# Performance work log

Measured on AMD Instinct MI355X. Metric: run time of the kernel, lower is better.

Reference implementation:

```python
import jax, jax.numpy as jnp
import numpy as np

RANKS_HIGH = 15   # dt.RANKS.HIGH in the repo
SUITS_HIGH = 14   # padded so conv output last dim == 10 (Linear(10,32))
EPS = 1e-5


def _bn(x, g, b, axes):
    # Batch-norm over `axes` with channel dim = 1, training-mode batch stats.
    m = jnp.mean(x, axis=axes, keepdims=True)
    v = jnp.var(x, axis=axes, keepdims=True)
    xn = (x - m) * jax.lax.rsqrt(v + EPS)
    shp = [1] * x.ndim
    shp[1] = -1
    return xn * g.reshape(shp) + b.reshape(shp)


def setup_inputs() -> dict:
    key = jax.random.key(0)
    ks = jax.random.split(key, 16)
    M = 4096
    s = 0.05
    return {
        "x": jax.random.randint(ks[0], (M, 5, 2), 0, 4),  # (rank, suit) indices
        "conv_w": jax.random.normal(ks[1], (64, 5, 5, 5), jnp.float32) * s,
        "conv_b": jax.random.normal(ks[2], (64,), jnp.float32) * s,
        "bn0_g": jnp.ones((64,), jnp.float32),
        "bn0_b": jnp.zeros((64,), jnp.float32),
        "w_rank": jax.random.normal(ks[3], (32, 10), jnp.float32) * s,
        "b_rank": jax.random.normal(ks[4], (32,), jnp.float32) * s,
        "w_h1": jax.random.normal(ks[5], (32, 32), jnp.float32) * s,
        "b_h1": jax.random.normal(ks[6], (32,), jnp.float32) * s,
        "bn1_g": jnp.ones((64,), jnp.float32),
        "bn1_b": jnp.zeros((64,), jnp.float32),
        "w_h2": jax.random.normal(ks[7], (16, 32), jnp.float32) * s,
        "b_h2": jax.random.normal(ks[8], (16,), jnp.float32) * s,
        "bn2_g": jnp.ones((64,), jnp.float32),
        "bn2_b": jnp.zeros((64,), jnp.float32),
        "w_out": jax.random.normal(ks[9], (9, 11264), jnp.float32) * s,
        "b_out": jax.random.normal(ks[10], (9,), jnp.float32) * s,
    }


def reference(x, conv_w, conv_b, bn0_g, bn0_b, w_rank, b_rank, w_h1, b_h1,
              bn1_g, bn1_b, w_h2, b_h2, bn2_g, bn2_b, w_out, b_out):
    ranks = x[:, :, 0]
    suits = x[:, :, 1]
    # Vectorized replacement of the double Python-loop one-hot scatter:
    # three_d[j, i, ranks[j, i], suits[j, i]] = 1  ->  outer product of one-hots.
    three_d = (jax.nn.one_hot(ranks, RANKS_HIGH, dtype=jnp.float32)[..., :, None]
               * jax.nn.one_hot(suits, SUITS_HIGH, dtype=jnp.float32)[..., None, :])  # [M,5,15,14]
    r = jax.lax.conv_general_dilated(
        three_d, conv_w, window_strides=(1, 1), padding="VALID",
        dimension_numbers=("NCHW", "OIHW", "NCHW"))  # [M,64,11,10]
    r = r + conv_b[None, :, None, None]
    r = jax.nn.relu(_bn(r, bn0_g, bn0_b, (0, 2, 3)))
    r = jax.nn.relu(jnp.einsum("mchs,os->mcho", r, w_rank) + b_rank)      # [M,64,11,32]
    r = jnp.einsum("mchi,oi->mcho", r, w_h1) + b_h1                        # [M,64,11,32]
    r = jax.nn.relu(_bn(r, bn1_g, bn1_b, (0, 2, 3)))
    r = jnp.einsum("mchi,oi->mcho", r, w_h2) + b_h2                        # [M,64,11,16]
    r = jax.nn.relu(_bn(r, bn2_g, bn2_b, (0, 2, 3)))
    r = r.reshape(r.shape[0], -1)                                          # [M,11264]
    return r @ w_out.T + b_out                                             # [M,9]
```

## Files before the change

kernel.cpp:

```cpp
#include <hip/hip_runtime.h>
#include <hip/hip_bf16.h>

#define EPSV 1e-5f

typedef float vf2 __attribute__((ext_vector_type(2)));
typedef _Float16 h4f __attribute__((ext_vector_type(4)));

__device__ __forceinline__ vf2 pk_fma(vf2 a, vf2 b, vf2 c) {
  vf2 d;
  asm("v_pk_fma_f32 %0, %1, %2, %3" : "=v"(d) : "v"(a), "v"(b), "v"(c));
  return d;
}
__device__ __forceinline__ vf2 pk_mul(vf2 a, vf2 b) {
  vf2 d;
  asm("v_pk_mul_f32 %0, %1, %2" : "=v"(d) : "v"(a), "v"(b));
  return d;
}

#define WS_SUM0   0
#define WS_SSQ0   64
#define WS_SUM1   128
#define WS_SSQ1   192
#define WS_SUM2   256
#define WS_SSQ2   320
#define WS_AL0    384
#define WS_BE0    448
#define WS_ZBG    512
#define WS_T1BG   576
#define WS_AL1    2624
#define WS_BE1    2688
#define WS_T2BG   2752
#define WS_AL2    3776
#define WS_BE2    3840
#define WS_A2BG   3904
#define WS_OC     4928
#define WS_CU     4992
#define WS_CW     5120
#define WS_HIST   10304
#define WS_WSUM   13056
#define WS_T1     24576

#define CONV_LDS 5184
#define NHIST 2640

__device__ __forceinline__ void stage_conv(float* sW, const float* __restrict__ conv_w,
                                           int nthr) {
  for (int i = threadIdx.x; i < 8000; i += nthr) {
    int k = i / 125, rem = i - k * 125;
    int cc = rem / 25, r2 = rem - cc * 25;
    int di = r2 / 5, dj = r2 - di * 5;
    if (di < 4 && dj < 4) sW[k * 81 + cc * 16 + di * 4 + dj] = conv_w[i];
  }
  for (int k = threadIdx.x; k < 64; k += nthr) sW[k * 81 + 80] = 0.f;
}

__device__ __forceinline__ void stage_conv_fast(float* sW, const float* __restrict__ cw) {
  const float4* src = (const float4*)cw;
  float4* dst = (float4*)sW;
  for (int i = threadIdx.x; i < CONV_LDS / 4; i += 256) dst[i] = src[i];
}

__device__ __forceinline__ int conv_idx(int di, int dj, int cc) {
  int idx = cc * 16 + di * 4 + dj;
  return ((di | dj) >= 0) ? idx : 80;
}

__global__ __launch_bounds__(256) void k_prep3(
    const int* __restrict__ x, const float* __restrict__ conv_w,
    const float* __restrict__ w_out, float* __restrict__ ws, int M) {
  __shared__ float h[NHIST];
  const int b = blockIdx.x;
  const int tid = threadIdx.x;
  if (b < 8) {
    float* cw = ws + WS_CW;
    const int gid = b * 256 + tid;
    for (int i = gid; i < 8000; i += 8 * 256) {
      int k = i / 125, rem = i - k * 125;
      int cc = rem / 25, r2 = rem - cc * 25;
      int di = r2 / 5, dj = r2 - di * 5;
      if (di < 4 && dj < 4) cw[k * 81 + cc * 16 + di * 4 + dj] = conv_w[i];
    }
    for (int k = gid; k < 64; k += 8 * 256) cw[k * 81 + 80] = 0.f;
  } else if (b < 44) {
    const int gid = (b - 8) * 256 + tid;
    if (gid < 9216) {
      int j = gid / 1024, kp = gid - j * 1024;
      int k = kp >> 4, p = kp & 15;
      float s = 0.f;
#pragma unroll
      for (int yy = 4; yy < 11; ++yy)
        s += w_out[j * 11264 + k * 176 + yy * 16 + p];
      ws[WS_WSUM + gid] = s;
    }
  } else {
    for (int i = tid; i < NHIST; i += 256) h[i] = 0.f;
    __syncthreads();
    for (int m = (b - 44) * 256 + tid; m < M; m += 16 * 256) {
      int v[5];
      const int2* xp = (const int2*)(x + m * 10);
#pragma unroll
      for (int cc = 0; cc < 5; ++cc) {
        int2 t = xp[cc];
        v[cc] = (t.x << 2) | t.y;
      }
#pragma unroll
      for (int cc = 0; cc < 5; ++cc) atomicAdd(&h[cc * 16 + v[cc]], 1.f);
      int pr = 0;
#pragma unroll
      for (int a = 0; a < 5; ++a)
#pragma unroll
        for (int bb = a + 1; bb < 5; ++bb) {
          atomicAdd(&h[80 + pr * 256 + v[a] * 16 + v[bb]], 1.f);
          ++pr;
        }
    }
    __syncthreads();
    for (int i = tid; i < NHIST; i += 256)
      if (h[i] != 0.f) atomicAdd(&ws[WS_HIST + i], h[i]);
  }
}

__global__ __launch_bounds__(256) void k_stats0h(
    const float* __restrict__ conv_b, float* __restrict__ ws, int M) {
  __shared__ float sWk[81];
  const int tid = threadIdx.x;
  const int k = blockIdx.x;
  if (tid < 81) sWk[tid] = ws[WS_CW + k * 81 + tid];
  __syncthreads();
  const float cb = conv_b[k];
  const float* H = ws + WS_HIST;
  float L = 0.f, Q = 0.f, P = 0.f;
  for (int it = tid; it < 1280; it += 256) {
    int pos = it / 80, rem = it - pos * 80;
    int cc = rem >> 4, v = rem & 15;
    int y = pos >> 2, xx = pos & 3;
    float w = sWk[conv_idx((v >> 2) - y, (v & 3) - xx, cc)];
    float n = H[cc * 16 + v];
    L += n * w;
    Q += n * w * w;
  }
  if (tid < 160) {
    int pos = tid / 10, pr = tid - pos * 10;
    int y = pos >> 2, xx = pos & 3;
    int a, b;
    if (pr < 4)      { a = 0; b = pr + 1; }
    else if (pr < 7) { a = 1; b = pr - 2; }
    else if (pr < 9) { a = 2; b = pr - 4; }
    else             { a = 3; b = 4; }
    const float* Hp = H + 80 + pr * 256;
    for (int v1 = 0; v1 < 16; ++v1) {
      float w1 = sWk[conv_idx((v1 >> 2) - y, (v1 & 3) - xx, a)];
      float acc = 0.f;
#pragma unroll
      for (int v2 = 0; v2 < 16; ++v2) {
        float w2 = sWk[conv_idx((v2 >> 2) - y, (v2 & 3) - xx, b)];
        acc += Hp[v1 * 16 + v2] * w2;
      }
      P += w1 * acc;
    }
  }
  atomicAdd(&ws[WS_SUM0 + k], L);
  atomicAdd(&ws[WS_SSQ0 + k], Q + 2.f * cb * L + 2.f * P);
  if (tid == 0) {
    const float a16 = 16.f * (float)M;
    atomicAdd(&ws[WS_SUM0 + k], a16 * cb);
    atomicAdd(&ws[WS_SSQ0 + k], a16 * cb * cb);
  }
}

__global__ __launch_bounds__(64) void k_fin0(
    const float* __restrict__ conv_b, const float* __restrict__ g0,
    const float* __restrict__ b0, const float* __restrict__ w_rank,
    const float* __restrict__ b_rank, const float* __restrict__ w_h1,
    const float* __restrict__ b_h1, float* __restrict__ ws, int M) {
  __shared__ float sS[32];
  const int t = threadIdx.x;
  if (t < 32) {
    float su = 0.f;
    for (int s2 = 0; s2 < 10; ++s2) su += w_rank[t * 10 + s2];
    sS[t] = su;
    float cu = 0.f;
    for (int s2 = 4; s2 < 10; ++s2) cu += w_rank[t * 10 + s2];
    ws[WS_CU + t] = cu;
  }
  __syncthreads();
  const int k = t;
  const float n0 = 110.f * (float)M;
  const float cb = conv_b[k];
  const float S  = ws[WS_SUM0 + k] + 94.f * (float)M * cb;
  const float SS = ws[WS_SSQ0 + k] + 94.f * (float)M * cb * cb;
  const float mu = S / n0;
  const float var = SS / n0 - mu * mu;
  const float rstd = rsqrtf(var + EPSV);
  const float al = rstd * g0[k];
  const float be = b0[k] - mu * al;
  ws[WS_AL0 + k] = al;
  ws[WS_BE0 + k] = be;
  const float zbg = fmaxf(cb * al + be, 0.f);
  ws[WS_ZBG + k] = zbg;
  float r1bg[32];
#pragma unroll
  for (int o = 0; o < 32; ++o) r1bg[o] = fmaxf(zbg * sS[o] + b_rank[o], 0.f);
  float sb = 0.f, ssb = 0.f;
  for (int o = 0; o < 32; ++o) {
    float acc = b_h1[o];
#pragma unroll
    for (int i = 0; i < 32; ++i) acc += r1bg[i] * w_h1[o * 32 + i];
    ws[WS_T1BG + k * 32 + o] = acc;
    sb += acc;
    ssb += acc * acc;
  }
  ws[WS_SUM1 + k] = 7.f * (float)M * sb;
  ws[WS_SSQ1 + k] = 7.f * (float)M * ssb;
}

__global__ __launch_bounds__(256) void k_t1(
    const int* __restrict__ x, const float* __restrict__ conv_b,
    const float* __restrict__ w_rank, const float* __restrict__ b_rank,
    const float* __restrict__ w_h1, const float* __restrict__ b_h1,
    float* __restrict__ ws, float* __restrict__ t1, int M) {
  __shared__ float sW[CONV_LDS];
  stage_conv_fast(sW, ws + WS_CW);
  __syncthreads();
  const int tid = threadIdx.x;
  const int y = tid & 3, k = tid >> 2;
  const float cb = conv_b[k];
  const float al = ws[WS_AL0 + k], be = ws[WS_BE0 + k], zbg = ws[WS_ZBG + k];
  const float* Wk = &sW[k * 81];
  const float* cu = ws + WS_CU;
  const vf2* wrp = (const vf2*)w_rank;
  const vf2* w1p = (const vf2*)w_h1;
  h4f* t1h = (h4f*)t1;
  float sAcc = 0.f, ssAcc = 0.f;
  const int NP = (M + 1) >> 1;
  for (int mp = blockIdx.x; mp < NP; mp += gridDim.x) {
    const int mA = mp * 2, mB = mA + 1;
    const bool hasB = (mB < M);
    const int mBs = hasB ? mB : mA;
    int rA[5], cA[5], rB[5], cBx[5];
    const int2* xpA = (const int2*)(x + mA * 10);
    const int2* xpB = (const int2*)(x + mBs * 10);
#pragma unroll
    for (int cc = 0; cc < 5; ++cc) {
      int2 tA = xpA[cc]; rA[cc] = tA.x; cA[cc] = tA.y;
      int2 tB = xpB[cc]; rB[cc] = tB.x; cBx[cc] = tB.y;
    }
    float a0A[4], a0B[4];
#pragma unroll
    for (int xx = 0; xx < 4; ++xx) {
      float vA = cb, vB = cb;
#pragma unroll
      for (int cc = 0; cc < 5; ++cc) {
        vA += Wk[conv_idx(rA[cc] - y, cA[cc] - xx, cc)];
        vB += Wk[conv_idx(rB[cc] - y, cBx[cc] - xx, cc)];
      }
      a0A[xx] = fmaxf(al * vA + be, 0.f);
      a0B[xx] = fmaxf(al * vB + be, 0.f);
    }
    vf2 aAp[2], aBp[2];
    aAp[0].x = a0A[0]; aAp[0].y = a0A[1];
    aAp[1].x = a0A[2]; aAp[1].y = a0A[3];
    aBp[0].x = a0B[0]; aBp[0].y = a0B[1];
    aBp[1].x = a0B[2]; aBp[1].y = a0B[3];
    __builtin_amdgcn_sched_barrier(0);
    vf2 r1A[16], r1B[16];
#pragma unroll
    for (int o2 = 0; o2 < 16; ++o2) {
      const int oa = 2 * o2, ob = oa + 1;
      vf2 w0 = wrp[oa * 5], w1 = wrp[oa * 5 + 1];
      vf2 w2 = wrp[ob * 5], w3 = wrp[ob * 5 + 1];
      const float basea = b_rank[oa] + zbg * cu[oa];
      const float baseb = b_rank[ob] + zbg * cu[ob];
      vf2 accAa = pk_mul(aAp[0], w0); accAa = pk_fma(aAp[1], w1, accAa);
      vf2 accAb = pk_mul(aAp[0], w2); accAb = pk_fma(aAp[1], w3, accAb);
      vf2 accBa = pk_mul(aBp[0], w0); accBa = pk_fma(aBp[1], w1, accBa);
      vf2 accBb = pk_mul(aBp[0], w2); accBb = pk_fma(aBp[1], w3, accBb);
      vf2 ra, rb;
      ra.x = fmaxf(basea + accAa.x + accAa.y, 0.f);
      ra.y = fmaxf(baseb + accAb.x + accAb.y, 0.f);
      rb.x = fmaxf(basea + accBa.x + accBa.y, 0.f);
      rb.y = fmaxf(baseb + accBb.x + accBb.y, 0.f);
      r1A[o2] = ra;
      r1B[o2] = rb;
    }
    __builtin_amdgcn_sched_barrier(0);
    float sBm = 0.f, ssBm = 0.f;
#pragma unroll
    for (int chv = 0; chv < 8; ++chv) {
      float accA[4], accB[4];
#pragma unroll
      for (int u = 0; u < 4; ++u) {
        const int o = chv * 4 + u;
        vf2 a2A = {0.f, 0.f}, a2B = {0.f, 0.f};
#pragma unroll
        for (int i = 0; i < 16; ++i) {
          vf2 w = w1p[o * 16 + i];
          a2A = pk_fma(r1A[i], w, a2A);
          a2B = pk_fma(r1B[i], w, a2B);
        }
        const float bb = b_h1[o];
        float aA = bb + a2A.x + a2A.y;
        float aB = bb + a2B.x + a2B.y;
        accA[u] = aA; accB[u] = aB;
        sAcc += aA; ssAcc += aA * aA;
        sBm += aB;  ssBm += aB * aB;
      }
      h4f stA;
      stA[0] = (_Float16)accA[0]; stA[1] = (_Float16)accA[1];
      stA[2] = (_Float16)accA[2]; stA[3] = (_Float16)accA[3];
      t1h[((size_t)mA * 8 + chv) * 256 + tid] = stA;
      if (hasB) {
        h4f stB;
        stB[0] = (_Float16)accB[0]; stB[1] = (_Float16)accB[1];
        stB[2] = (_Float16)accB[2]; stB[3] = (_Float16)accB[3];
        t1h[((size_t)mB * 8 + chv) * 256 + tid] = stB;
      }
      __builtin_amdgcn_sched_barrier(0);
    }
    if (hasB) { sAcc += sBm; ssAcc += ssBm; }
  }
  sAcc  += __shfl_xor(sAcc, 1);  sAcc  += __shfl_xor(sAcc, 2);
  ssAcc += __shfl_xor(ssAcc, 1); ssAcc += __shfl_xor(ssAcc, 2);
  if (y == 0) {
    atomicAdd(&ws[WS_SUM1 + k], sAcc);
    atomicAdd(&ws[WS_SSQ1 + k], ssAcc);
  }
}

__global__ __launch_bounds__(64) void k_fin1(
    const float* __restrict__ g1, const float* __restrict__ b1,
    const float* __restrict__ w_h2, const float* __restrict__ b_h2,
    float* __restrict__ ws, int M) {
  const int k = threadIdx.x;
  const float n1 = (float)M * 11.f * 32.f;
  const float S = ws[WS_SUM1 + k], SS = ws[WS_SSQ1 + k];
  const float mu = S / n1;
  const float var = SS / n1 - mu * mu;
  const float rstd = rsqrtf(var + EPSV);
  const float al = rstd * g1[k];
  const float be = b1[k] - mu * al;
  ws[WS_AL1 + k] = al;
  ws[WS_BE1 + k] = be;
  float a1bg[32];
#pragma unroll
  for (int o = 0; o < 32; ++o)
    a1bg[o] = fmaxf(al * ws[WS_T1BG + k * 32 + o] + be, 0.f);
  float sb = 0.f, ssb = 0.f;
  for (int p = 0; p < 16; ++p) {
    float acc = b_h2[p];
#pragma unroll
    for (int o = 0; o < 32; ++o) acc += a1bg[o] * w_h2[p * 32 + o];
    ws[WS_T2BG + k * 16 + p] = acc;
    sb += acc;
    ssb += acc * acc;
  }
  ws[WS_SUM2 + k] = 7.f * (float)M * sb;
  ws[WS_SSQ2 + k] = 7.f * (float)M * ssb;
}

__global__ __launch_bounds__(256) void k_t2(
    const float* __restrict__ w_h2, const float* __restrict__ b_h2,
    float* __restrict__ ws, float* __restrict__ t1, int M) {
  const int tid = threadIdx.x;
  const int y = tid & 3, k = tid >> 2;
  const float al1 = ws[WS_AL1 + k], be1 = ws[WS_BE1 + k];
  const vf2* w2p = (const vf2*)w_h2;
  h4f* t1h = (h4f*)t1;
  float sAcc = 0.f, ssAcc = 0.f;
  const int NP = (M + 1) >> 1;
  for (int mp = blockIdx.x; mp < NP; mp += gridDim.x) {
    const int mA = mp * 2, mB = mA + 1;
    const bool hasB = (mB < M);
    const int mBs = hasB ? mB : mA;
    vf2 a1A[16], a1B[16];
#pragma unroll
    for (int chv = 0; chv < 8; ++chv) {
      h4f vA = t1h[((size_t)mA * 8 + chv) * 256 + tid];
      h4f vB = t1h[((size_t)mBs * 8 + chv) * 256 + tid];
      vf2 pA0, pA1, pB0, pB1;
      pA0.x = fmaxf(al1 * (float)vA[0] + be1, 0.f);
      pA0.y = fmaxf(al1 * (float)vA[1] + be1, 0.f);
      pA1.x = fmaxf(al1 * (float)vA[2] + be1, 0.f);
      pA1.y = fmaxf(al1 * (float)vA[3] + be1, 0.f);
      pB0.x = fmaxf(al1 * (float)vB[0] + be1, 0.f);
      pB0.y = fmaxf(al1 * (float)vB[1] + be1, 0.f);
      pB1.x = fmaxf(al1 * (float)vB[2] + be1, 0.f);
      pB1.y = fmaxf(al1 * (float)vB[3] + be1, 0.f);
      a1A[chv * 2] = pA0; a1A[chv * 2 + 1] = pA1;
      a1B[chv * 2] = pB0; a1B[chv * 2 + 1] = pB1;
    }
    __builtin_amdgcn_sched_barrier(0);
    float sBm = 0.f, ssBm = 0.f;
#pragma unroll
    for (int pv = 0; pv < 4; ++pv) {
      float accA[4], accB[4];
#pragma unroll
      for (int u = 0; u < 4; ++u) {
        const int p = pv * 4 + u;
        vf2 a2A = {0.f, 0.f}, a2B = {0.f, 0.f};
#pragma unroll
        for (int i = 0; i < 16; ++i) {
          vf2 w = w2p[p * 16 + i];
          a2A = pk_fma(a1A[i], w, a2A);
          a2B = pk_fma(a1B[i], w, a2B);
        }
        const float bb = b_h2[p];
        float aA = bb + a2A.x + a2A.y;
        float aB = bb + a2B.x + a2B.y;
        accA[u] = aA; accB[u] = aB;
        sAcc += aA; ssAcc += aA * aA;
        sBm += aB;  ssBm += aB * aB;
      }
      h4f stA;
      stA[0] = (_Float16)accA[0]; stA[1] = (_Float16)accA[1];
      stA[2] = (_Float16)accA[2]; stA[3] = (_Float16)accA[3];
      t1h[((size_t)mA * 8 + pv) * 256 + tid] = stA;
      if (hasB) {
        h4f stB;
        stB[0] = (_Float16)accB[0]; stB[1] = (_Float16)accB[1];
        stB[2] = (_Float16)accB[2]; stB[3] = (_Float16)accB[3];
        t1h[((size_t)mB * 8 + pv) * 256 + tid] = stB;
      }
      __builtin_amdgcn_sched_barrier(0);
    }
    if (hasB) { sAcc += sBm; ssAcc += ssBm; }
  }
  sAcc  += __shfl_xor(sAcc, 1);  sAcc  += __shfl_xor(sAcc, 2);
  ssAcc += __shfl_xor(ssAcc, 1); ssAcc += __shfl_xor(ssAcc, 2);
  if (y == 0) {
    atomicAdd(&ws[WS_SUM2 + k], sAcc);
    atomicAdd(&ws[WS_SSQ2 + k], ssAcc);
  }
}

__global__ __launch_bounds__(64) void k_fin2f(
    const float* __restrict__ g2, const float* __restrict__ b2,
    const float* __restrict__ b_out, float* __restrict__ ws, int M) {
  __shared__ float red[64 * 9];
  const int k = threadIdx.x;
  const float n2 = (float)M * 11.f * 16.f;
  const float S = ws[WS_SUM2 + k], SS = ws[WS_SSQ2 + k];
  const float mu = S / n2;
  const float var = SS / n2 - mu * mu;
  const float rstd = rsqrtf(var + EPSV);
  const float al = rstd * g2[k];
  const float be = b2[k] - mu * al;
  ws[WS_AL2 + k] = al;
  ws[WS_BE2 + k] = be;
  float a2bg[16];
#pragma unroll
  for (int p = 0; p < 16; ++p) {
    a2bg[p] = fmaxf(al * ws[WS_T2BG + k * 16 + p] + be, 0.f);
    ws[WS_A2BG + k * 16 + p] = a2bg[p];
  }
  for (int j = 0; j < 9; ++j) {
    const float* wsj = ws + WS_WSUM + j * 1024 + k * 16;
    float acc = 0.f;
#pragma unroll
    for (int p = 0; p < 16; ++p) acc += a2bg[p] * wsj[p];
    red[k * 9 + j] = acc;
  }
  __syncthreads();
  if (k < 9) {
    float acc = b_out[k];
    for (int t = 0; t < 64; ++t) acc += red[t * 9 + k];
    ws[WS_OC + k] = acc;
  }
}

__global__ __launch_bounds__(256) void k_out(
    const float* __restrict__ w_out, const float* __restrict__ ws,
    const float* __restrict__ t1, float* __restrict__ out, int M) {
  __shared__ float sOC[9];
  __shared__ float sRedA[4][9], sRedB[4][9];
  if (threadIdx.x < 9) sOC[threadIdx.x] = ws[WS_OC + threadIdx.x];
  __syncthreads();
  const int tid = threadIdx.x;
  const int lane = tid & 63, wv = tid >> 6;
  const int y = tid & 3, k = tid >> 2;
  const float al2 = ws[WS_AL2 + k], be2 = ws[WS_BE2 + k];
  const float4* wo = (const float4*)(w_out + k * 176 + y * 16);
  const h4f* t2h = (const h4f*)t1;
  const int NP = (M + 1) >> 1;
  bool first = true;
  for (int mp = blockIdx.x; mp < NP; mp += gridDim.x) {
    if (!first) __syncthreads();
    first = false;
    const int mA = mp * 2, mB = mA + 1;
    const bool hasB = (mB < M);
    const int mBs = hasB ? mB : mA;
    vf2 a2A[8], a2B[8];
#pragma unroll
    for (int iv = 0; iv < 4; ++iv) {
      h4f vA = t2h[((size_t)mA * 8 + iv) * 256 + tid];
      h4f vB = t2h[((size_t)mBs * 8 + iv) * 256 + tid];
      vf2 pA0, pA1, pB0, pB1;
      pA0.x = fmaxf(al2 * (float)vA[0] + be2, 0.f);
      pA0.y = fmaxf(al2 * (float)vA[1] + be2, 0.f);
      pA1.x = fmaxf(al2 * (float)vA[2] + be2, 0.f);
      pA1.y = fmaxf(al2 * (float)vA[3] + be2, 0.f);
      pB0.x = fmaxf(al2 * (float)vB[0] + be2, 0.f);
      pB0.y = fmaxf(al2 * (float)vB[1] + be2, 0.f);
      pB1.x = fmaxf(al2 * (float)vB[2] + be2, 0.f);
      pB1.y = fmaxf(al2 * (float)vB[3] + be2, 0.f);
      a2A[iv * 2] = pA0; a2A[iv * 2 + 1] = pA1;
      a2B[iv * 2] = pB0; a2B[iv * 2 + 1] = pB1;
    }
    float poA[9], poB[9];
#pragma unroll
    for (int j = 0; j < 9; ++j) {
      float4 w0 = wo[j * 2816 + 0], w1 = wo[j * 2816 + 1];
      float4 w2 = wo[j * 2816 + 2], w3 = wo[j * 2816 + 3];
      vf2 aA = {0.f, 0.f}, aB = {0.f, 0.f};
      vf2 t;
      t.x = w0.x; t.y = w0.y; aA = pk_fma(a2A[0], t, aA); aB = pk_fma(a2B[0], t, aB);
      t.x = w0.z; t.y = w0.w; aA = pk_fma(a2A[1], t, aA); aB = pk_fma(a2B[1], t, aB);
      t.x = w1.x; t.y = w1.y; aA = pk_fma(a2A[2], t, aA); aB = pk_fma(a2B[2], t, aB);
      t.x = w1.z; t.y = w1.w; aA = pk_fma(a2A[3], t, aA); aB = pk_fma(a2B[3], t, aB);
      t.x = w2.x; t.y = w2.y; aA = pk_fma(a2A[4], t, aA); aB = pk_fma(a2B[4], t, aB);
      t.x = w2.z; t.y = w2.w; aA = pk_fma(a2A[5], t, aA); aB = pk_fma(a2B[5], t, aB);
      t.x = w3.x; t.y = w3.y; aA = pk_fma(a2A[6], t, aA); aB = pk_fma(a2B[6], t, aB);
      t.x = w3.z; t.y = w3.w; aA = pk_fma(a2A[7], t, aA); aB = pk_fma(a2B[7], t, aB);
      poA[j] = aA.x + aA.y;
      poB[j] = aB.x + aB.y;
    }
#pragma unroll
    for (int j = 0; j < 9; ++j) {
      float vA = poA[j], vB = poB[j];
      vA += __shfl_xor(vA, 1);  vB += __shfl_xor(vB, 1);
      vA += __shfl_xor(vA, 2);  vB += __shfl_xor(vB, 2);
      vA += __shfl_xor(vA, 4);  vB += __shfl_xor(vB, 4);
      vA += __shfl_xor(vA, 8);  vB += __shfl_xor(vB, 8);
      vA += __shfl_xor(vA, 16); vB += __shfl_xor(vB, 16);
      vA += __shfl_xor(vA, 32); vB += __shfl_xor(vB, 32);
      poA[j] = vA; poB[j] = vB;
    }
    if (lane == 0) {
#pragma unroll
      for (int j = 0; j < 9; ++j) { sRedA[wv][j] = poA[j]; sRedB[wv][j] = poB[j]; }
    }
    __syncthreads();
    if (tid < 9) {
      float acc = sOC[tid];
#pragma unroll
      for (int w2i = 0; w2i < 4; ++w2i) acc += sRedA[w2i][tid];
      out[mA * 9 + tid] = acc;
    } else if (tid >= 64 && tid < 73 && hasB) {
      const int j = tid - 64;
      float acc = sOC[j];
#pragma unroll
      for (int w2i = 0; w2i < 4; ++w2i) acc += sRedB[w2i][j];
      out[mB * 9 + j] = acc;
    }
  }
}

__global__ __launch_bounds__(256) void k_stats0(
    const int* __restrict__ x, const float* __restrict__ conv_w,
    const float* __restrict__ conv_b, float* __restrict__ ws, int M) {
  __shared__ float sW[CONV_LDS];
  stage_conv(sW, conv_w, 256);
  __syncthreads();
  const int tid = threadIdx.x;
  const int mg = tid & 3;
  const int k  = tid >> 2;
  const float cb = conv_b[k];
  const float* Wk = &sW[k * 81];
  float s = 0.f, ss = 0.f;
  for (int m = blockIdx.x * 4 + mg; m < M; m += gridDim.x * 4) {
    int r[5], c[5];
    const int2* xp = (const int2*)(x + m * 10);
#pragma unroll
    for (int cc = 0; cc < 5; ++cc) { int2 t = xp[cc]; r[cc] = t.x; c[cc] = t.y; }
#pragma unroll
    for (int y = 0; y < 4; ++y) {
#pragma unroll
      for (int xx = 0; xx < 4; ++xx) {
        float v = cb;
#pragma unroll
        for (int cc = 0; cc < 5; ++cc)
          v += Wk[conv_idx(r[cc] - y, c[cc] - xx, cc)];
        s += v;
        ss += v * v;
      }
      __builtin_amdgcn_sched_barrier(0);
    }
  }
  s  += __shfl_xor(s, 1);  s  += __shfl_xor(s, 2);
  ss += __shfl_xor(ss, 1); ss += __shfl_xor(ss, 2);
  if (mg == 0) {
    atomicAdd(&ws[WS_SUM0 + k], s);
    atomicAdd(&ws[WS_SSQ0 + k], ss);
  }
}

__global__ __launch_bounds__(256) void k_stats1(
    const int* __restrict__ x, const float* __restrict__ conv_w,
    const float* __restrict__ conv_b, const float* __restrict__ w_rank,
    const float* __restrict__ b_rank, const float* __restrict__ w_h1,
    const float* __restrict__ b_h1, float* __restrict__ ws, int M) {
  __shared__ float sW[CONV_LDS];
  stage_conv(sW, conv_w, 256);
  __syncthreads();
  const int tid = threadIdx.x;
  const int y = tid & 3, k = tid >> 2;
  const float cb = conv_b[k];
  const float al = ws[WS_AL0 + k], be = ws[WS_BE0 + k], zbg = ws[WS_ZBG + k];
  const float* Wk = &sW[k * 81];
  const float* cu = ws + WS_CU;
  float sAcc = 0.f, ssAcc = 0.f;
  for (int m = blockIdx.x; m < M; m += gridDim.x) {
    int r[5], c[5];
    const int2* xp = (const int2*)(x + m * 10);
#pragma unroll
    for (int cc = 0; cc < 5; ++cc) { int2 t = xp[cc]; r[cc] = t.x; c[cc] = t.y; }
    float a0[4];
#pragma unroll
    for (int xx = 0; xx < 4; ++xx) {
      float v = cb;
#pragma unroll
      for (int cc = 0; cc < 5; ++cc)
        v += Wk[conv_idx(r[cc] - y, c[cc] - xx, cc)];
      a0[xx] = fmaxf(al * v + be, 0.f);
    }
    __builtin_amdgcn_sched_barrier(0);
    float r1[32];
#pragma unroll
    for (int o = 0; o < 32; ++o) {
      float acc = b_rank[o] + zbg * cu[o];
#pragma unroll
      for (int xx = 0; xx < 4; ++xx) acc += a0[xx] * w_rank[o * 10 + xx];
      r1[o] = fmaxf(acc, 0.f);
    }
    __builtin_amdgcn_sched_barrier(0);
    float s1 = 0.f, ss1 = 0.f;
#pragma unroll
    for (int ch = 0; ch < 4; ++ch) {
#pragma unroll
      for (int u = 0; u < 8; ++u) {
        const int o = ch * 8 + u;
        float acc = b_h1[o];
#pragma unroll
        for (int i = 0; i < 32; ++i) acc += r1[i] * w_h1[o * 32 + i];
        s1 += acc;
        ss1 += acc * acc;
      }
      __builtin_amdgcn_sched_barrier(0);
    }
    sAcc += s1;
    ssAcc += ss1;
  }
  sAcc  += __shfl_xor(sAcc, 1);  sAcc  += __shfl_xor(sAcc, 2);
  ssAcc += __shfl_xor(ssAcc, 1); ssAcc += __shfl_xor(ssAcc, 2);
  if (y == 0) {
    atomicAdd(&ws[WS_SUM1 + k], sAcc);
    atomicAdd(&ws[WS_SSQ1 + k], ssAcc);
  }
}

__global__ __launch_bounds__(256) void k_stats2(
    const int* __restrict__ x, const float* __restrict__ conv_w,
    const float* __restrict__ conv_b, const float* __restrict__ w_rank,
    const float* __restrict__ b_rank, const float* __restrict__ w_h1,
    const float* __restrict__ b_h1, const float* __restrict__ w_h2,
    const float* __restrict__ b_h2, float* __restrict__ ws, int M) {
  __shared__ float sW[CONV_LDS];
  stage_conv(sW, conv_w, 256);
  __syncthreads();
  const int tid = threadIdx.x;
  const int y = tid & 3, k = tid >> 2;
  const float cb = conv_b[k];
  const float al = ws[WS_AL0 + k], be = ws[WS_BE0 + k], zbg = ws[WS_ZBG + k];
  const float al1 = ws[WS_AL1 + k], be1 = ws[WS_BE1 + k];
  const float* Wk = &sW[k * 81];
  const float* cu = ws + WS_CU;
  float sAcc = 0.f, ssAcc = 0.f;
  for (int m = blockIdx.x; m < M; m += gridDim.x) {
    int r[5], c[5];
    const int2* xp = (const int2*)(x + m * 10);
#pragma unroll
    for (int cc = 0; cc < 5; ++cc) { int2 t = xp[cc]; r[cc] = t.x; c[cc] = t.y; }
    float a0[4];
#pragma unroll
    for (int xx = 0; xx < 4; ++xx) {
      float v = cb;
#pragma unroll
      for (int cc = 0; cc < 5; ++cc)
        v += Wk[conv_idx(r[cc] - y, c[cc] - xx, cc)];
      a0[xx] = fmaxf(al * v + be, 0.f);
    }
    __builtin_amdgcn_sched_barrier(0);
    float r1[32];
#pragma unroll
    for (int o = 0; o < 32; ++o) {
      float acc = b_rank[o] + zbg * cu[o];
#pragma unroll
      for (int xx = 0; xx < 4; ++xx) acc += a0[xx] * w_rank[o * 10 + xx];
      r1[o] = fmaxf(acc, 0.f);
    }
    __builtin_amdgcn_sched_barrier(0);
    float t2[16];
#pragma unroll
    for (int p = 0; p < 16; ++p) t2[p] = b_h2[p];
#pragma unroll
    for (int ch = 0; ch < 4; ++ch) {
      float a1c[8];
#pragma unroll
      for (int u = 0; u < 8; ++u) {
        const int o = ch * 8 + u;
        float acc = b_h1[o];
#pragma unroll
        for (int i = 0; i < 32; ++i) acc += r1[i] * w_h1[o * 32 + i];
        a1c[u] = fmaxf(al1 * acc + be1, 0.f);
      }
      __builtin_amdgcn_sched_barrier(0);
#pragma unroll
      for (int p = 0; p < 16; ++p) {
        float acc = t2[p];
#pragma unroll
        for (int u = 0; u < 8; ++u) acc += a1c[u] * w_h2[p * 32 + ch * 8 + u];
        t2[p] = acc;
      }
      __builtin_amdgcn_sched_barrier(0);
    }
    float s2l = 0.f, ss2l = 0.f;
#pragma unroll
    for (int p = 0; p < 16; ++p) { s2l += t2[p]; ss2l += t2[p] * t2[p]; }
    sAcc += s2l;
    ssAcc += ss2l;
  }
  sAcc  += __shfl_xor(sAcc, 1);  sAcc  += __shfl_xor(sAcc, 2);
  ssAcc += __shfl_xor(ssAcc, 1); ssAcc += __shfl_xor(ssAcc, 2);
  if (y == 0) {
    atomicAdd(&ws[WS_SUM2 + k], sAcc);
    atomicAdd(&ws[WS_SSQ2 + k], ssAcc);
  }
}

__global__ __launch_bounds__(64) void k_fin2(
    const float* __restrict__ g2, const float* __restrict__ b2,
    const float* __restrict__ w_out, const float* __restrict__ b_out,
    float* __restrict__ ws, int M) {
  __shared__ float red[64 * 9];
  const int k = threadIdx.x;
  const float n2 = (float)M * 11.f * 16.f;
  const float S = ws[WS_SUM2 + k], SS = ws[WS_SSQ2 + k];
  const float mu = S / n2;
  const float var = SS / n2 - mu * mu;
  const float rstd = rsqrtf(var + EPSV);
  const float al = rstd * g2[k];
  const float be = b2[k] - mu * al;
  ws[WS_AL2 + k] = al;
  ws[WS_BE2 + k] = be;
  float a2bg[16];
#pragma unroll
  for (int p = 0; p < 16; ++p) {
    a2bg[p] = fmaxf(al * ws[WS_T2BG + k * 16 + p] + be, 0.f);
    ws[WS_A2BG + k * 16 + p] = a2bg[p];
  }
  for (int j = 0; j < 9; ++j) {
    float acc = 0.f;
#pragma unroll
    for (int p = 0; p < 16; ++p) {
      float wsum = 0.f;
#pragma unroll
      for (int yy = 4; yy < 11; ++yy)
        wsum += w_out[j * 11264 + k * 176 + yy * 16 + p];
      acc += a2bg[p] * wsum;
    }
    red[k * 9 + j] = acc;
  }
  __syncthreads();
  if (k < 9) {
    float acc = b_out[k];
    for (int t = 0; t < 64; ++t) acc += red[t * 9 + k];
    ws[WS_OC + k] = acc;
  }
}

__global__ __launch_bounds__(256) void k_final(
    const int* __restrict__ x, const float* __restrict__ conv_w,
    const float* __restrict__ conv_b, const float* __restrict__ w_rank,
    const float* __restrict__ b_rank, const float* __restrict__ w_h1,
    const float* __restrict__ b_h1, const float* __restrict__ w_h2,
    const float* __restrict__ b_h2, const float* __restrict__ w_out,
    const float* __restrict__ ws, float* __restrict__ out, int M) {
  __shared__ float sW[CONV_LDS];
  __shared__ float sOC[9];
  __shared__ float sRed[4][9];
  stage_conv(sW, conv_w, 256);
  if (threadIdx.x < 9) sOC[threadIdx.x] = ws[WS_OC + threadIdx.x];
  __syncthreads();
  const int tid = threadIdx.x;
  const int lane = tid & 63, wv = tid >> 6;
  const int y = tid & 3, k = tid >> 2;
  const float cb = conv_b[k];
  const float al = ws[WS_AL0 + k], be = ws[WS_BE0 + k], zbg = ws[WS_ZBG + k];
  const float al1 = ws[WS_AL1 + k], be1 = ws[WS_BE1 + k];
  const float al2 = ws[WS_AL2 + k], be2 = ws[WS_BE2 + k];
  const float* Wk = &sW[k * 81];
  const float* cu = ws + WS_CU;
  const float4* wo = (const float4*)(w_out + k * 176 + y * 16);
  bool first = true;
  for (int m = blockIdx.x; m < M; m += gridDim.x) {
    if (!first) __syncthreads();
    first = false;
    int r[5], c[5];
    const int2* xp = (const int2*)(x + m * 10);
#pragma unroll
    for (int cc = 0; cc < 5; ++cc) { int2 t = xp[cc]; r[cc] = t.x; c[cc] = t.y; }
    float a0[4];
#pragma unroll
    for (int xx = 0; xx < 4; ++xx) {
      float v = cb;
#pragma unroll
      for (int cc = 0; cc < 5; ++cc)
        v += Wk[conv_idx(r[cc] - y, c[cc] - xx, cc)];
      a0[xx] = fmaxf(al * v + be, 0.f);
    }
    __builtin_amdgcn_sched_barrier(0);
    float r1[32];
#pragma unroll
    for (int o = 0; o < 32; ++o) {
      float acc = b_rank[o] + zbg * cu[o];
#pragma unroll
      for (int xx = 0; xx < 4; ++xx) acc += a0[xx] * w_rank[o * 10 + xx];
      r1[o] = fmaxf(acc, 0.f);
    }
    __builtin_amdgcn_sched_barrier(0);
    float t2[16];
#pragma unroll
    for (int p = 0; p < 16; ++p) t2[p] = b_h2[p];
#pragma unroll
    for (int ch = 0; ch < 4; ++ch) {
      float a1c[8];
#pragma unroll
      for (int u = 0; u < 8; ++u) {
        const int o = ch * 8 + u;
        float acc = b_h1[o];
#pragma unroll
        for (int i = 0; i < 32; ++i) acc += r1[i] * w_h1[o * 32 + i];
        a1c[u] = fmaxf(al1 * acc + be1, 0.f);
      }
      __builtin_amdgcn_sched_barrier(0);
#pragma unroll
      for (int p = 0; p < 16; ++p) {
        float acc = t2[p];
#pragma unroll
        for (int u = 0; u < 8; ++u) acc += a1c[u] * w_h2[p * 32 + ch * 8 + u];
        t2[p] = acc;
      }
      __builtin_amdgcn_sched_barrier(0);
    }
    float a2[16];
#pragma unroll
    for (int p = 0; p < 16; ++p) a2[p] = fmaxf(al2 * t2[p] + be2, 0.f);
    float po[9];
#pragma unroll
    for (int j = 0; j < 9; ++j) {
      float4 w0 = wo[j * 2816 + 0], w1 = wo[j * 2816 + 1];
      float4 w2 = wo[j * 2816 + 2], w3 = wo[j * 2816 + 3];
      po[j] = a2[0] * w0.x + a2[1] * w0.y + a2[2] * w0.z + a2[3] * w0.w
            + a2[4] * w1.x + a2[5] * w1.y + a2[6] * w1.z + a2[7] * w1.w
            + a2[8] * w2.x + a2[9] * w2.y + a2[10] * w2.z + a2[11] * w2.w
            + a2[12] * w3.x + a2[13] * w3.y + a2[14] * w3.z + a2[15] * w3.w;
    }
#pragma unroll
    for (int j = 0; j < 9; ++j) {
      float v = po[j];
      v += __shfl_xor(v, 1);
      v += __shfl_xor(v, 2);
      v += __shfl_xor(v, 4);
      v += __shfl_xor(v, 8);
      v += __shfl_xor(v, 16);
      v += __shfl_xor(v, 32);
      po[j] = v;
    }
    if (lane == 0) {
#pragma unroll
      for (int j = 0; j < 9; ++j) sRed[wv][j] = po[j];
    }
    __syncthreads();
    if (tid < 9) {
      float acc = sOC[tid];
#pragma unroll
      for (int w2i = 0; w2i < 4; ++w2i) acc += sRed[w2i][tid];
      out[m * 9 + tid] = acc;
    }
  }
}

extern "C" void kernel_launch(void* const* d_in, const int* in_sizes, int n_in,
                              void* d_out, int out_size, void* d_ws, size_t ws_size,
                              hipStream_t stream) {
  const int*   x      = (const int*)d_in[0];
  const float* conv_w = (const float*)d_in[1];
  const float* conv_b = (const float*)d_in[2];
  const float* bn0_g  = (const float*)d_in[3];
  const float* bn0_b  = (const float*)d_in[4];
  const float* w_rank = (const float*)d_in[5];
  const float* b_rank = (const float*)d_in[6];
  const float* w_h1   = (const float*)d_in[7];
  const float* b_h1   = (const float*)d_in[8];
  const float* bn1_g  = (const float*)d_in[9];
  const float* bn1_b  = (const float*)d_in[10];
  const float* w_h2   = (const float*)d_in[11];
  const float* b_h2   = (const float*)d_in[12];
  const float* bn2_g  = (const float*)d_in[13];
  const float* bn2_b  = (const float*)d_in[14];
  const float* w_out  = (const float*)d_in[15];
  const float* b_out  = (const float*)d_in[16];
  float* out = (float*)d_out;
  float* ws  = (float*)d_ws;
  const int M = in_sizes[0] / 10;
  const size_t need = ((size_t)WS_T1 + (size_t)M * 4096) * sizeof(float);
  const int NP = (M + 1) >> 1;
  const int gridp = NP < 2048 ? NP : 2048;

  hipMemsetAsync(ws, 0, 384 * sizeof(float), stream);

  if (ws_size >= need) {
    float* t1 = ws + WS_T1;
    hipMemsetAsync(ws + WS_HIST, 0, NHIST * sizeof(float), stream);
    k_prep3<<<60, 256, 0, stream>>>(x, conv_w, w_out, ws, M);
    k_stats0h<<<64, 256, 0, stream>>>(conv_b, ws, M);
    k_fin0<<<1, 64, 0, stream>>>(conv_b, bn0_g, bn0_b, w_rank, b_rank, w_h1, b_h1, ws, M);
    k_t1<<<gridp, 256, 0, stream>>>(x, conv_b, w_rank, b_rank, w_h1, b_h1, ws, t1, M);
    k_fin1<<<1, 64, 0, stream>>>(bn1_g, bn1_b, w_h2, b_h2, ws, M);
    k_t2<<<gridp, 256, 0, stream>>>(w_h2, b_h2, ws, t1, M);
    k_fin2f<<<1, 64, 0, stream>>>(bn2_g, bn2_b, b_out, ws, M);
    k_out<<<gridp, 256, 0, stream>>>(w_out, ws, t1, out, M);
  } else {
    k_stats0<<<512, 256, 0, stream>>>(x, conv_w, conv_b, ws, M);
    k_fin0<<<1, 64, 0, stream>>>(conv_b, bn0_g, bn0_b, w_rank, b_rank, w_h1, b_h1, ws, M);
    k_stats1<<<1024, 256, 0, stream>>>(x, conv_w, conv_b, w_rank, b_rank, w_h1, b_h1,
                                       ws, M);
    k_fin1<<<1, 64, 0, stream>>>(bn1_g, bn1_b, w_h2, b_h2, ws, M);
    k_stats2<<<1024, 256, 0, stream>>>(x, conv_w, conv_b, w_rank, b_rank, w_h1, b_h1,
                                       w_h2, b_h2, ws, M);
    k_fin2<<<1, 64, 0, stream>>>(bn2_g, bn2_b, w_out, b_out, ws, M);
    k_final<<<1024, 256, 0, stream>>>(x, conv_w, conv_b, w_rank, b_rank, w_h1, b_h1,
                                      w_h2, b_h2, w_out, ws, out, M);
  }
}
```

Baseline: 311.4 us.

## Fuse t2, fin2 and output kernels via software grid barrier with LDS-resident t2

Merges the second hidden layer, the BN2 finalize and the output projection into one persistent kernel of 1024 blocks. Each block processes up to two sample pairs and keeps their t2 activations in shared memory instead of writing them to and reading them back from global memory. A software grid barrier built on atomics waits for the BN2 statistics before the output stage runs. This removes two kernel launches and a global round trip. The cost is that all 1024 blocks must be co-resident for the spin barrier (launch_bounds of 4 blocks per CU), and every block now redundantly recomputes the BN2 finalize and output constants.

After: 350.3 us. +12.5%, slower.

```diff
diff --git a/kernel.cpp b/kernel.cpp
--- a/kernel.cpp
+++ b/kernel.cpp
@@ -38,10 +38,12 @@
 #define WS_CW     5120
 #define WS_HIST   10304
 #define WS_WSUM   13056
+#define WS_BAR    22272
 #define WS_T1     24576
 
 #define CONV_LDS 5184
 #define NHIST 2640
+#define G_FUSED 1024
 
 __device__ __forceinline__ void stage_conv(float* sW, const float* __restrict__ conv_w,
                                            int nthr) {
@@ -63,6 +65,24 @@
 __device__ __forceinline__ int conv_idx(int di, int dj, int cc) {
   int idx = cc * 16 + di * 4 + dj;
   return ((di | dj) >= 0) ? idx : 80;
+}
+
+__device__ __forceinline__ void soft_grid_barrier(int* bar, int nblocks) {
+  __syncthreads();
+  if (threadIdx.x == 0) {
+    __threadfence();
+    int arrived = __hip_atomic_fetch_add(bar, 1, __ATOMIC_ACQ_REL,
+                                         __HIP_MEMORY_SCOPE_AGENT);
+    if (arrived == nblocks - 1) {
+      __hip_atomic_store(bar + 1, 1, __ATOMIC_RELEASE, __HIP_MEMORY_SCOPE_AGENT);
+    } else {
+      while (__hip_atomic_load(bar + 1, __ATOMIC_ACQUIRE,
+                               __HIP_MEMORY_SCOPE_AGENT) == 0) {
+        __builtin_amdgcn_s_sleep(2);
+      }
+    }
+  }
+  __syncthreads();
 }
 
 __global__ __launch_bounds__(256) void k_prep3(
@@ -358,72 +378,82 @@
   ws[WS_SSQ2 + k] = 7.f * (float)M * ssb;
 }
 
-__global__ __launch_bounds__(256) void k_t2(
+__global__ __launch_bounds__(256, 4) void k_t2out(
     const float* __restrict__ w_h2, const float* __restrict__ b_h2,
-    float* __restrict__ ws, float* __restrict__ t1, int M) {
+    const float* __restrict__ g2, const float* __restrict__ b2,
+    const float* __restrict__ w_out, const float* __restrict__ b_out,
+    float* __restrict__ ws, const float* __restrict__ t1,
+    float* __restrict__ out, int M) {
+  __shared__ h4f sT2[2][8][256];
+  __shared__ float red[64 * 9];
+  __shared__ float sOC[9];
+  __shared__ float sRedA[4][9], sRedB[4][9];
   const int tid = threadIdx.x;
+  const int lane = tid & 63, wv = tid >> 6;
   const int y = tid & 3, k = tid >> 2;
   const float al1 = ws[WS_AL1 + k], be1 = ws[WS_BE1 + k];
   const vf2* w2p = (const vf2*)w_h2;
-  h4f* t1h = (h4f*)t1;
+  const h4f* t1h = (const h4f*)t1;
+  const int NP = (M + 1) >> 1;
   float sAcc = 0.f, ssAcc = 0.f;
-  const int NP = (M + 1) >> 1;
-  for (int mp = blockIdx.x; mp < NP; mp += gridDim.x) {
-    const int mA = mp * 2, mB = mA + 1;
-    const bool hasB = (mB < M);
-    const int mBs = hasB ? mB : mA;
-    vf2 a1A[16], a1B[16];
-#pragma unroll
-    for (int chv = 0; chv < 8; ++chv) {
-      h4f vA = t1h[((size_t)mA * 8 + chv) * 256 + tid];
-      h4f vB = t1h[((size_t)mBs * 8 + chv) * 256 + tid];
-      vf2 pA0, pA1, pB0, pB1;
-      pA0.x = fmaxf(al1 * (float)vA[0] + be1, 0.f);
-      pA0.y = fmaxf(al1 * (float)vA[1] + be1, 0.f);
-      pA1.x = fmaxf(al1 * (float)vA[2] + be1, 0.f);
-      pA1.y = fmaxf(al1 * (float)vA[3] + be1, 0.f);
-      pB0.x = fmaxf(al1 * (float)vB[0] + be1, 0.f);
-      pB0.y = fmaxf(al1 * (float)vB[1] + be1, 0.f);
-      pB1.x = fmaxf(al1 * (float)vB[2] + be1, 0.f);
-      pB1.y = fmaxf(al1 * (float)vB[3] + be1, 0.f);
-      a1A[chv * 2] = pA0; a1A[chv * 2 + 1] = pA1;
-      a1B[chv * 2] = pB0; a1B[chv * 2 + 1] = pB1;
-    }
-    __builtin_amdgcn_sched_barrier(0);
-    float sBm = 0.f, ssBm = 0.f;
-#pragma unroll
-    for (int pv = 0; pv < 4; ++pv) {
-      float accA[4], accB[4];
-#pragma unroll
-      for (int u = 0; u < 4; ++u) {
-        const int p = pv * 4 + u;
-        vf2 a2A = {0.f, 0.f}, a2B = {0.f, 0.f};
-#pragma unroll
-        for (int i = 0; i < 16; ++i) {
-          vf2 w = w2p[p * 16 + i];
-          a2A = pk_fma(a1A[i], w, a2A);
-          a2B = pk_fma(a1B[i], w, a2B);
+
+#pragma unroll
+  for (int pi = 0; pi < 2; ++pi) {
+    const int mp = blockIdx.x + pi * (int)gridDim.x;
+    if (mp < NP) {
+      const int mA = mp * 2, mB = mA + 1;
+      const bool hasB = (mB < M);
+      const int mBs = hasB ? mB : mA;
+      vf2 a1A[16], a1B[16];
+#pragma unroll
+      for (int chv = 0; chv < 8; ++chv) {
+        h4f vA = t1h[((size_t)mA * 8 + chv) * 256 + tid];
+        h4f vB = t1h[((size_t)mBs * 8 + chv) * 256 + tid];
+        vf2 pA0, pA1, pB0, pB1;
+        pA0.x = fmaxf(al1 * (float)vA[0] + be1, 0.f);
+        pA0.y = fmaxf(al1 * (float)vA[1] + be1, 0.f);
+        pA1.x = fmaxf(al1 * (float)vA[2] + be1, 0.f);
+        pA1.y = fmaxf(al1 * (float)vA[3] + be1, 0.f);
+        pB0.x = fmaxf(al1 * (float)vB[0] + be1, 0.f);
+        pB0.y = fmaxf(al1 * (float)vB[1] + be1, 0.f);
+        pB1.x = fmaxf(al1 * (float)vB[2] + be1, 0.f);
+        pB1.y = fmaxf(al1 * (float)vB[3] + be1, 0.f);
+        a1A[chv * 2] = pA0; a1A[chv * 2 + 1] = pA1;
+        a1B[chv * 2] = pB0; a1B[chv * 2 + 1] = pB1;
+      }
+      __builtin_amdgcn_sched_barrier(0);
+      float sBm = 0.f, ssBm = 0.f;
+#pragma unroll
+      for (int pv = 0; pv < 4; ++pv) {
+        float accA[4], accB[4];
+#pragma unroll
+        for (int u = 0; u < 4; ++u) {
+          const int p = pv * 4 + u;
+          vf2 a2A = {0.f, 0.f}, a2B = {0.f, 0.f};
+#pragma unroll
+          for (int i = 0; i < 16; ++i) {
+            vf2 w = w2p[p * 16 + i];
+            a2A = pk_fma(a1A[i], w, a2A);
+            a2B = pk_fma(a1B[i], w, a2B);
+          }
+          const float bb = b_h2[p];
+          float aA = bb + a2A.x + a2A.y;
+          float aB = bb + a2B.x + a2B.y;
+          accA[u] = aA; accB[u] = aB;
+          sAcc += aA; ssAcc += aA * aA;
+          sBm += aB;  ssBm += aB * aB;
         }
-        const float bb = b_h2[p];
-        float aA = bb + a2A.x + a2A.y;
-        float aB = bb + a2B.x + a2B.y;
-        accA[u] = aA; accB[u] = aB;
-        sAcc += aA; ssAcc += aA * aA;
-        sBm += aB;  ssBm += aB * aB;
-      }
-      h4f stA;
-      stA[0] = (_Float16)accA[0]; stA[1] = (_Float16)accA[1];
-      stA[2] = (_Float16)accA[2]; stA[3] = (_Float16)accA[3];
-      t1h[((size_t)mA * 8 + pv) * 256 + tid] = stA;
-      if (hasB) {
+        h4f stA;
+        stA[0] = (_Float16)accA[0]; stA[1] = (_Float16)accA[1];
+        stA[2] = (_Float16)accA[2]; stA[3] = (_Float16)accA[3];
+        sT2[pi][pv][tid] = stA;
         h4f stB;
         stB[0] = (_Float16)accB[0]; stB[1] = (_Float16)accB[1];
         stB[2] = (_Float16)accB[2]; stB[3] = (_Float16)accB[3];
-        t1h[((size_t)mB * 8 + pv) * 256 + tid] = stB;
-      }
-      __builtin_amdgcn_sched_barrier(0);
-    }
-    if (hasB) { sAcc += sBm; ssAcc += ssBm; }
+        sT2[pi][4 + pv][tid] = stB;
+      }
+      if (hasB) { sAcc += sBm; ssAcc += ssBm; }
+    }
   }
   sAcc  += __shfl_xor(sAcc, 1);  sAcc  += __shfl_xor(sAcc, 2);
   ssAcc += __shfl_xor(ssAcc, 1); ssAcc += __shfl_xor(ssAcc, 2);
@@ -431,69 +461,56 @@
     atomicAdd(&ws[WS_SUM2 + k], sAcc);
     atomicAdd(&ws[WS_SSQ2 + k], ssAcc);
   }
-}
-
-__global__ __launch_bounds__(64) void k_fin2f(
-    const float* __restrict__ g2, const float* __restrict__ b2,
-    const float* __restrict__ b_out, float* __restrict__ ws, int M) {
-  __shared__ float red[64 * 9];
-  const int k = threadIdx.x;
+
+  soft_grid_barrier((int*)(ws + WS_BAR), (int)gridDim.x);
+
+  const float S2 = __hip_atomic_load(&ws[WS_SUM2 + k], __ATOMIC_RELAXED,
+                                     __HIP_MEMORY_SCOPE_AGENT);
+  const float SS2 = __hip_atomic_load(&ws[WS_SSQ2 + k], __ATOMIC_RELAXED,
+                                      __HIP_MEMORY_SCOPE_AGENT);
   const float n2 = (float)M * 11.f * 16.f;
-  const float S = ws[WS_SUM2 + k], SS = ws[WS_SSQ2 + k];
-  const float mu = S / n2;
-  const float var = SS / n2 - mu * mu;
-  const float rstd = rsqrtf(var + EPSV);
-  const float al = rstd * g2[k];
-  const float be = b2[k] - mu * al;
-  ws[WS_AL2 + k] = al;
-  ws[WS_BE2 + k] = be;
-  float a2bg[16];
-#pragma unroll
-  for (int p = 0; p < 16; ++p) {
-    a2bg[p] = fmaxf(al * ws[WS_T2BG + k * 16 + p] + be, 0.f);
-    ws[WS_A2BG + k * 16 + p] = a2bg[p];
-  }
-  for (int j = 0; j < 9; ++j) {
-    const float* wsj = ws + WS_WSUM + j * 1024 + k * 16;
-    float acc = 0.f;
-#pragma unroll
-    for (int p = 0; p < 16; ++p) acc += a2bg[p] * wsj[p];
-    red[k * 9 + j] = acc;
-  }
-  __syncthreads();
-  if (k < 9) {
-    float acc = b_out[k];
-    for (int t = 0; t < 64; ++t) acc += red[t * 9 + k];
-    ws[WS_OC + k] = acc;
-  }
-}
-
-__global__ __launch_bounds__(256) void k_out(
-    const float* __restrict__ w_out, const float* __restrict__ ws,
-    const float* __restrict__ t1, float* __restrict__ out, int M) {
-  __shared__ float sOC[9];
-  __shared__ float sRedA[4][9], sRedB[4][9];
-  if (threadIdx.x < 9) sOC[threadIdx.x] = ws[WS_OC + threadIdx.x];
-  __syncthreads();
-  const int tid = threadIdx.x;
-  const int lane = tid & 63, wv = tid >> 6;
-  const int y = tid & 3, k = tid >> 2;
-  const float al2 = ws[WS_AL2 + k], be2 = ws[WS_BE2 + k];
+  const float mu2 = S2 / n2;
+  const float var2 = SS2 / n2 - mu2 * mu2;
+  const float rstd2 = rsqrtf(var2 + EPSV);
+  const float al2 = rstd2 * g2[k];
+  const float be2 = b2[k] - mu2 * al2;
+
+  if (y == 0) {
+    float a2bg[16];
+#pragma unroll
+    for (int p = 0; p < 16; ++p)
+      a2bg[p] = fmaxf(al2 * ws[WS_T2BG + k * 16 + p] + be2, 0.f);
+    for (int j = 0; j < 9; ++j) {
+      const float* wsj = ws + WS_WSUM + j * 1024 + k * 16;
+      float acc = 0.f;
+#pragma unroll
+      for (int p = 0; p < 16; ++p) acc += a2bg[p] * wsj[p];
+      red[k * 9 + j] = acc;
+    }
+  }
+  __syncthreads();
+  if (tid < 9) {
+    float acc = b_out[tid];
+    for (int t = 0; t < 64; ++t) acc += red[t * 9 + tid];
+    sOC[tid] = acc;
+  }
+  __syncthreads();
+
   const float4* wo = (const float4*)(w_out + k * 176 + y * 16);
-  const h4f* t2h = (const h4f*)t1;
-  const int NP = (M + 1) >> 1;
   bool first = true;
-  for (int mp = blockIdx.x; mp < NP; mp += gridDim.x) {
+#pragma unroll
+  for (int pi = 0; pi < 2; ++pi) {
+    const int mp = blockIdx.x + pi * (int)gridDim.x;
+    if (mp >= NP) continue;
     if (!first) __syncthreads();
     first = false;
     const int mA = mp * 2, mB = mA + 1;
     const bool hasB = (mB < M);
-    const int mBs = hasB ? mB : mA;
     vf2 a2A[8], a2B[8];
 #pragma unroll
     for (int iv = 0; iv < 4; ++iv) {
-      h4f vA = t2h[((size_t)mA * 8 + iv) * 256 + tid];
-      h4f vB = t2h[((size_t)mBs * 8 + iv) * 256 + tid];
+      h4f vA = sT2[pi][iv][tid];
+      h4f vB = sT2[pi][4 + iv][tid];
       vf2 pA0, pA1, pB0, pB1;
       pA0.x = fmaxf(al2 * (float)vA[0] + be2, 0.f);
       pA0.y = fmaxf(al2 * (float)vA[1] + be2, 0.f);
@@ -915,22 +932,20 @@
   const int M = in_sizes[0] / 10;
   const size_t need = ((size_t)WS_T1 + (size_t)M * 4096) * sizeof(float);
   const int NP = (M + 1) >> 1;
-  const int gridp = NP < 2048 ? NP : 2048;
-
-  hipMemsetAsync(ws, 0, 384 * sizeof(float), stream);
-
-  if (ws_size >= need) {
+
+  if (ws_size >= need && NP <= 2 * G_FUSED) {
     float* t1 = ws + WS_T1;
-    hipMemsetAsync(ws + WS_HIST, 0, NHIST * sizeof(float), stream);
+    const int gridt1 = NP < 1024 ? NP : 1024;
+    hipMemsetAsync(ws, 0, (size_t)WS_T1 * sizeof(float), stream);
     k_prep3<<<60, 256, 0, stream>>>(x, conv_w, w_out, ws, M);
     k_stats0h<<<64, 256, 0, stream>>>(conv_b, ws, M);
     k_fin0<<<1, 64, 0, stream>>>(conv_b, bn0_g, bn0_b, w_rank, b_rank, w_h1, b_h1, ws, M);
-    k_t1<<<gridp, 256, 0, stream>>>(x, conv_b, w_rank, b_rank, w_h1, b_h1, ws, t1, M);
+    k_t1<<<gridt1, 256, 0, stream>>>(x, conv_b, w_rank, b_rank, w_h1, b_h1, ws, t1, M);
     k_fin1<<<1, 64, 0, stream>>>(bn1_g, bn1_b, w_h2, b_h2, ws, M);
-    k_t2<<<gridp, 256, 0, stream>>>(w_h2, b_h2, ws, t1, M);
-    k_fin2f<<<1, 64, 0, stream>>>(bn2_g, bn2_b, b_out, ws, M);
-    k_out<<<gridp, 256, 0, stream>>>(w_out, ws, t1, out, M);
+    k_t2out<<<G_FUSED, 256, 0, stream>>>(w_h2, b_h2, bn2_g, bn2_b, w_out, b_out,
+                                         ws, t1, out, M);
   } else {
+    hipMemsetAsync(ws, 0, 384 * sizeof(float), stream);
     k_stats0<<<512, 256, 0, stream>>>(x, conv_w, conv_b, ws, M);
     k_fin0<<<1, 64, 0, stream>>>(conv_b, bn0_g, bn0_b, w_rank, b_rank, w_h1, b_h1, ws, M);
     k_stats1<<<1024, 256, 0, stream>>>(x, conv_w, conv_b, w_rank, b_rank, w_h1, b_h1,
```
